# Performance work log

Hardware: AMD Instinct MI355X
Metric: run time of the kernel (lower is better)

Reference implementation:

```python
import jax, jax.numpy as jnp
import numpy as np

B = 16384
MV = 512   # movie_vector_size
UV = 512   # user_vector_size
NM = 16    # num_dense_movie_embeddings
NU = 16    # num_dense_user_embeddings
DS = 16    # dense_embedding_size
MLP = [256, 128, 1]


def setup_inputs() -> dict:
    key = jax.random.key(0)
    ks = jax.random.split(key, 12)
    inp = {
        'movie_vectors': jax.random.normal(ks[0], (B, MV), jnp.float32),
        'user_vectors': jax.random.normal(ks[1], (B, UV), jnp.float32),
        # embedding towers: Linear(in, DS*N + 1), stored as [in, out]
        'Wm': jax.random.normal(ks[2], (MV, DS * NM + 1), jnp.float32) * (1.0 / np.sqrt(MV)),
        'bm': jax.random.normal(ks[3], (DS * NM + 1,), jnp.float32) * 0.01,
        'Wu': jax.random.normal(ks[4], (UV, DS * NU + 1), jnp.float32) * (1.0 / np.sqrt(UV)),
        'bu': jax.random.normal(ks[5], (DS * NU + 1,), jnp.float32) * 0.01,
    }
    d_in = (NM + NU) * DS  # 512
    dims = [d_in] + MLP
    for i in range(len(MLP)):
        inp[f'W{i+1}'] = jax.random.normal(ks[6 + 2*i], (dims[i], dims[i+1]), jnp.float32) * (1.0 / np.sqrt(dims[i]))
        inp[f'b{i+1}'] = jax.random.normal(ks[7 + 2*i], (dims[i+1],), jnp.float32) * 0.01
    return inp


def reference(movie_vectors, user_vectors, Wm, bm, Wu, bu, W1, b1, W2, b2, W3, b3):
    batch = movie_vectors.shape[0]
    movie_dense = movie_vectors @ Wm + bm          # [B, DS*NM+1]
    user_dense = user_vectors @ Wu + bu            # [B, DS*NU+1]
    fm_additive = movie_dense[:, -1] + user_dense[:, -1]            # [B]
    m_split = movie_dense[:, :-1].reshape(batch, NM, DS)            # [B, NM, DS]
    u_split = user_dense[:, :-1].reshape(batch, NU, DS)             # [B, NU, DS]
    fm_interactions = jnp.einsum('bik,bjk->bij', m_split, u_split).reshape(batch, -1)  # [B, NM*NU]
    all_dense = jnp.concatenate([movie_dense[:, :-1], user_dense[:, :-1]], axis=-1)    # [B, (NM+NU)*DS]
    h = jax.nn.relu(all_dense @ W1 + b1)
    h = jax.nn.relu(h @ W2 + b2)
    mlp_out = h @ W3 + b3                                           # [B, 1]
    logit = mlp_out + fm_additive[:, None] + jnp.sum(fm_interactions, axis=-1, keepdims=True)
    return logit
```

## Files before the change

kernel.cpp:

```cpp
#include <hip/hip_runtime.h>


#define NTH 1024
#define RB  64

typedef __bf16 bf16x8 __attribute__((ext_vector_type(8)));
typedef float  f32x4  __attribute__((ext_vector_type(4)));

#define WS_WMF  0
#define WS_WUF  294912
#define WS_W1F  589824
#define WS_W2F  851968
#define WS_BIAS 917504

#define BPITCH  528
#define L_BST   0
#define L_DENSE 67584
#define L_FM    133120
#define L_ADD   141824
#define L_OUT   142336
#define LDSB    142592

__device__ __forceinline__ unsigned short f2bf(float f) {
  unsigned u = __builtin_bit_cast(unsigned, f);
  u += 0x7FFFu + ((u >> 16) & 1u);
  return (unsigned short)(u >> 16);
}

__device__ __forceinline__ f32x4 mfma_bf16(bf16x8 a, bf16x8 b, f32x4 c) {
  return __builtin_amdgcn_mfma_f32_16x16x32_bf16(a, b, c, 0, 0, 0);
}

extern "C" __global__ __launch_bounds__(256) void deepfm_prep(
    const float* __restrict__ Wm, const float* __restrict__ bm,
    const float* __restrict__ Wu, const float* __restrict__ bu,
    const float* __restrict__ W1, const float* __restrict__ W2,
    const float* __restrict__ b3, char* __restrict__ ws) {
  const int unit = blockIdx.x * 4 + (threadIdx.x >> 6);
  if (unit >= 897) return;
  const int l = threadIdx.x & 63;
  const int fi = l & 15, q = l >> 4;
  unsigned short h[8];
  if (unit < 576) {
    const int t = unit / 288, rem = unit % 288;
    const int kg = rem / 18, ft = rem % 18;
    const float* W = t ? Wu : Wm;
    char* outp = ws + (t ? WS_WUF : WS_WMF);
    const int f = ft * 16 + fi;
#pragma unroll
    for (int e = 0; e < 8; ++e) {
      const int k = kg * 32 + q * 8 + e;
      float val;
      if (f < 256) val = W[k * 257 + f];
      else if (f < 272) {
        float s = 0.f;
#pragma unroll
        for (int i = 0; i < 16; ++i) s += W[k * 257 + i * 16 + (f - 256)];
        val = s;
      } else if (f == 272) val = W[k * 257 + 256];
      else val = 0.f;
      h[e] = f2bf(val);
    }
    uint4 o;
    o.x = h[0] | ((unsigned)h[1] << 16); o.y = h[2] | ((unsigned)h[3] << 16);
    o.z = h[4] | ((unsigned)h[5] << 16); o.w = h[6] | ((unsigned)h[7] << 16);
    *(uint4*)(outp + (((kg * 18 + ft) * 64 + l) << 4)) = o;
  } else if (unit < 832) {
    const int bb = unit - 576;
    const int kg = bb / 16, ft = bb % 16;
    const int f = ft * 16 + fi;
#pragma unroll
    for (int e = 0; e < 8; ++e) h[e] = f2bf(W1[(kg * 32 + q * 8 + e) * 256 + f]);
    uint4 o;
    o.x = h[0] | ((unsigned)h[1] << 16); o.y = h[2] | ((unsigned)h[3] << 16);
    o.z = h[4] | ((unsigned)h[5] << 16); o.w = h[6] | ((unsigned)h[7] << 16);
    *(uint4*)(ws + WS_W1F + (((kg * 16 + ft) * 64 + l) << 4)) = o;
  } else if (unit < 896) {
    const int bb = unit - 832;
    const int kg = bb / 8, ft = bb % 8;
    const int f = ft * 16 + fi;
#pragma unroll
    for (int e = 0; e < 8; ++e) h[e] = f2bf(W2[(kg * 32 + q * 8 + e) * 128 + f]);
    uint4 o;
    o.x = h[0] | ((unsigned)h[1] << 16); o.y = h[2] | ((unsigned)h[3] << 16);
    o.z = h[4] | ((unsigned)h[5] << 16); o.w = h[6] | ((unsigned)h[7] << 16);
    *(uint4*)(ws + WS_W2F + (((kg * 8 + ft) * 64 + l) << 4)) = o;
  } else {
    float* aux = (float*)(ws + WS_BIAS);
    if (l < 16) {
      float s = 0.f;
      for (int i = 0; i < 16; ++i) s += bm[i * 16 + l];
      aux[l] = s;
    } else if (l < 32) {
      const int k = l - 16;
      float s = 0.f;
      for (int i = 0; i < 16; ++i) s += bu[i * 16 + k];
      aux[l] = s;
    } else if (l == 32) {
      aux[32] = bm[256] + bu[256] + b3[0];
    }
  }
}

extern "C" __global__ __launch_bounds__(NTH)
__attribute__((amdgpu_waves_per_eu(4, 4))) void deepfm_main(
    const float* __restrict__ movie, const float* __restrict__ user,
    const float* __restrict__ bm, const float* __restrict__ bu,
    const float* __restrict__ b1, const float* __restrict__ b2,
    const float* __restrict__ W3, const char* __restrict__ ws,
    float* __restrict__ out) {
  extern __shared__ __align__(16) char lds[];
  char* const bstage    = lds + L_BST;
  char* const densefrag = lds + L_DENSE;
  char* const h1frag    = lds + L_BST;
  float* const fmbuf    = (float*)(lds + L_FM);
  float* const addbuf   = (float*)(lds + L_ADD);
  float* const outpart  = (float*)(lds + L_OUT);

  const int tid = threadIdx.x;
  const int w   = tid >> 6;
  const int l   = tid & 63;
  const int cn  = l & 15;
  const int q   = l >> 4;
  const int row0 = blockIdx.x * RB;

  const int tw   = w >> 3;
  const int wi   = w & 7;
  const int axi  = wi & 1;
  const int axrt = wi >> 1;
  const int ftw  = w & 7;
  const int rth  = w >> 3;

  const int rot  = (int)blockIdx.x >> 3;
  const int hord = rot & 1;
  const int kk0  = (rot >> 1) & 7;
  const int p2r  = rot & 15;
  const int p3r  = rot & 7;

  const f32x4 zz = {0.f, 0.f, 0.f, 0.f};
  const float* auxb = (const float*)(ws + WS_BIAS);

  bf16x8 p2a;
  bf16x8 p3a;

  {
    const char* WF = ws + (tw ? WS_WUF : WS_WMF);
    const char* brow = bstage + tw * 64 * BPITCH;
    f32x4 a0r0 = zz, a0r1 = zz, a0r2 = zz, a0r3 = zz;
    f32x4 a1r0 = zz, a1r1 = zz, a1r2 = zz, a1r3 = zz;
    f32x4 axc = zz;

    const int h0 = hord, h1h = hord ^ 1;

#pragma unroll
    for (int p = 0; p < 8; ++p) {
      const int idx = p * 1024 + tid;
      const int rr = idx >> 6, f4 = idx & 63;
      const float* src = (rr >= 64) ? user : movie;
      const float4 v = *(const float4*)(src + (size_t)(row0 + (rr & 63)) * 512 +
                                        h0 * 256 + f4 * 4);
      uint2 o;
      o.x = f2bf(v.x) | ((unsigned)f2bf(v.y) << 16);
      o.y = f2bf(v.z) | ((unsigned)f2bf(v.w) << 16);
      *(uint2*)(bstage + rr * BPITCH + f4 * 8) = o;
    }
    __syncthreads();

    float4 pf[8];
#pragma unroll
    for (int p = 0; p < 8; ++p) {
      const int idx = p * 1024 + tid;
      const int rr = idx >> 6, f4 = idx & 63;
      const float* src = (rr >= 64) ? user : movie;
      pf[p] = *(const float4*)(src + (size_t)(row0 + (rr & 63)) * 512 +
                               h1h * 256 + f4 * 4);
    }
    uint2 pfc[8];

#pragma unroll
    for (int i = 0; i < 8; ++i) {
      const int kgl = (kk0 + i) & 7;
      const int kg  = h0 * 8 + kgl;
      const bf16x8 bf0 = *(const bf16x8*)(brow + cn * BPITCH + kgl * 64 + q * 16);
      const bf16x8 bf1 = *(const bf16x8*)(brow + (16 + cn) * BPITCH + kgl * 64 + q * 16);
      const bf16x8 bf2 = *(const bf16x8*)(brow + (32 + cn) * BPITCH + kgl * 64 + q * 16);
      const bf16x8 bf3 = *(const bf16x8*)(brow + (48 + cn) * BPITCH + kgl * 64 + q * 16);
      const bf16x8 A0 = *(const bf16x8*)(WF + (((kg * 18 + wi * 2 + 0) * 64 + l) << 4));
      const bf16x8 A1 = *(const bf16x8*)(WF + (((kg * 18 + wi * 2 + 1) * 64 + l) << 4));
      const bf16x8 AX = *(const bf16x8*)(WF + (((kg * 18 + 16 + axi) * 64 + l) << 4));
      __builtin_amdgcn_s_setprio(1);
      a0r0 = mfma_bf16(A0, bf0, a0r0);  a0r1 = mfma_bf16(A0, bf1, a0r1);
      a0r2 = mfma_bf16(A0, bf2, a0r2);  a0r3 = mfma_bf16(A0, bf3, a0r3);
      a1r0 = mfma_bf16(A1, bf0, a1r0);  a1r1 = mfma_bf16(A1, bf1, a1r1);
      a1r2 = mfma_bf16(A1, bf2, a1r2);  a1r3 = mfma_bf16(A1, bf3, a1r3);
      const bf16x8 bsel = (axrt == 0) ? bf0 : (axrt == 1) ? bf1
                        : (axrt == 2) ? bf2 : bf3;
      axc = mfma_bf16(AX, bsel, axc);
      __builtin_amdgcn_s_setprio(0);
      if (i >= 1) {
        const int j = i - 1;
        pfc[j].x = f2bf(pf[j].x) | ((unsigned)f2bf(pf[j].y) << 16);
        pfc[j].y = f2bf(pf[j].z) | ((unsigned)f2bf(pf[j].w) << 16);
      }
    }
    pfc[7].x = f2bf(pf[7].x) | ((unsigned)f2bf(pf[7].y) << 16);
    pfc[7].y = f2bf(pf[7].z) | ((unsigned)f2bf(pf[7].w) << 16);

    __syncthreads();

    bf16x8 A0c = *(const bf16x8*)(WF + ((((h1h * 8 + kk0) * 18 + wi * 2 + 0) * 64 + l) << 4));
    bf16x8 A1c = *(const bf16x8*)(WF + ((((h1h * 8 + kk0) * 18 + wi * 2 + 1) * 64 + l) << 4));

#pragma unroll
    for (int p = 0; p < 8; ++p) {
      const int idx = p * 1024 + tid;
      const int rr = idx >> 6, f4 = idx & 63;
      *(uint2*)(bstage + rr * BPITCH + f4 * 8) = pfc[p];
    }
    __syncthreads();

#pragma unroll
    for (int i = 0; i < 8; ++i) {
      const int kgl = (kk0 + i) & 7;
      const int kg  = h1h * 8 + kgl;
      const bf16x8 bf0 = *(const bf16x8*)(brow + cn * BPITCH + kgl * 64 + q * 16);
      const bf16x8 bf1 = *(const bf16x8*)(brow + (16 + cn) * BPITCH + kgl * 64 + q * 16);
      const bf16x8 bf2 = *(const bf16x8*)(brow + (32 + cn) * BPITCH + kgl * 64 + q * 16);
      const bf16x8 bf3 = *(const bf16x8*)(brow + (48 + cn) * BPITCH + kgl * 64 + q * 16);
      const bf16x8 AX = *(const bf16x8*)(WF + (((kg * 18 + 16 + axi) * 64 + l) << 4));
      bf16x8 A0n, A1n;
      if (i < 7) {
        const int nkg = h1h * 8 + ((kk0 + i + 1) & 7);
        A0n = *(const bf16x8*)(WF + (((nkg * 18 + wi * 2 + 0) * 64 + l) << 4));
        A1n = *(const bf16x8*)(WF + (((nkg * 18 + wi * 2 + 1) * 64 + l) << 4));
      } else {
        A0n = A0c; A1n = A1c;
      }
      __builtin_amdgcn_s_setprio(1);
      a0r0 = mfma_bf16(A0c, bf0, a0r0);  a0r1 = mfma_bf16(A0c, bf1, a0r1);
      a0r2 = mfma_bf16(A0c, bf2, a0r2);  a0r3 = mfma_bf16(A0c, bf3, a0r3);
      a1r0 = mfma_bf16(A1c, bf0, a1r0);  a1r1 = mfma_bf16(A1c, bf1, a1r1);
      a1r2 = mfma_bf16(A1c, bf2, a1r2);  a1r3 = mfma_bf16(A1c, bf3, a1r3);
      const bf16x8 bsel = (axrt == 0) ? bf0 : (axrt == 1) ? bf1
                        : (axrt == 2) ? bf2 : bf3;
      axc = mfma_bf16(AX, bsel, axc);
      __builtin_amdgcn_s_setprio(0);
      A0c = A0n; A1c = A1n;
    }

    p2a = *(const bf16x8*)(ws + WS_W1F + (((p2r * 16 + w) * 64 + l) << 4));

    const float* bt = tw ? bu : bm;
    const f32x4 accA[2][4] = {{a0r0, a0r1, a0r2, a0r3}, {a1r0, a1r1, a1r2, a1r3}};
#pragma unroll
    for (int s = 0; s < 2; ++s) {
      const int ft = wi * 2 + s;
      const int fb = ft * 16 + q * 4;
      const float g0 = bt[fb], g1 = bt[fb + 1], g2 = bt[fb + 2], g3 = bt[fb + 3];
      const int kd = tw * 256 + fb;
      const int kgd = kd >> 5, qd = (kd >> 3) & 3, ed = kd & 4;
#pragma unroll
      for (int rt = 0; rt < 4; ++rt) {
        const f32x4 v = accA[s][rt];
        uint2 p;
        p.x = f2bf(v[0] + g0) | ((unsigned)f2bf(v[1] + g1) << 16);
        p.y = f2bf(v[2] + g2) | ((unsigned)f2bf(v[3] + g3) << 16);
        *(uint2*)(densefrag + (((kgd * 4 + rt) * 64 + qd * 16 + cn) << 4) +
                  (ed ? 8 : 0)) = p;
      }
    }

    if (axi == 0) {
#pragma unroll
      for (int reg = 0; reg < 4; ++reg)
        fmbuf[(tw * 64 + axrt * 16 + cn) * 17 + (q * 4 + reg)] = axc[reg];
    } else if (q == 0) {
      addbuf[tw * 64 + axrt * 16 + cn] = axc[0];
    }
  }

  __syncthreads();

  if (tid < 64) {
    float p = 0.f;
#pragma unroll
    for (int k = 0; k < 16; ++k)
      p += (fmbuf[tid * 17 + k] + auxb[k]) *
           (fmbuf[(64 + tid) * 17 + k] + auxb[16 + k]);
    outpart[tid] = p + addbuf[tid] + addbuf[64 + tid] + auxb[32];
  }

  {
    const char* W1F = ws + WS_W1F;
    bf16x8 a0c = p2a;
    f32x4 r0 = zz, r1 = zz, r2 = zz, r3 = zz;
#pragma unroll
    for (int i = 0; i < 16; ++i) {
      const int kg = (p2r + i) & 15;
      const bf16x8 b0 = *(const bf16x8*)(densefrag + (((kg * 4 + 0) * 64 + l) << 4));
      const bf16x8 b1f = *(const bf16x8*)(densefrag + (((kg * 4 + 1) * 64 + l) << 4));
      const bf16x8 b2f = *(const bf16x8*)(densefrag + (((kg * 4 + 2) * 64 + l) << 4));
      const bf16x8 b3f = *(const bf16x8*)(densefrag + (((kg * 4 + 3) * 64 + l) << 4));
      bf16x8 a0n;
      if (i < 15) {
        const int nkg = (p2r + i + 1) & 15;
        a0n = *(const bf16x8*)(W1F + (((nkg * 16 + w) * 64 + l) << 4));
      } else {
        a0n = a0c;
      }
      __builtin_amdgcn_s_setprio(1);
      r0 = mfma_bf16(a0c, b0,  r0);
      r1 = mfma_bf16(a0c, b1f, r1);
      r2 = mfma_bf16(a0c, b2f, r2);
      r3 = mfma_bf16(a0c, b3f, r3);
      __builtin_amdgcn_s_setprio(0);
      a0c = a0n;
    }

    p3a = *(const bf16x8*)(ws + WS_W2F + (((p3r * 8 + ftw) * 64 + l) << 4));

    const f32x4 accA[4] = {r0, r1, r2, r3};
    const int fb = w * 16 + q * 4;
    const float g0 = b1[fb], g1 = b1[fb + 1], g2 = b1[fb + 2], g3 = b1[fb + 3];
    const int kgd = fb >> 5, qd = (fb >> 3) & 3, ed = fb & 4;
#pragma unroll
    for (int rt = 0; rt < 4; ++rt) {
      const f32x4 v = accA[rt];
      uint2 p;
      p.x = f2bf(fmaxf(v[0] + g0, 0.f)) | ((unsigned)f2bf(fmaxf(v[1] + g1, 0.f)) << 16);
      p.y = f2bf(fmaxf(v[2] + g2, 0.f)) | ((unsigned)f2bf(fmaxf(v[3] + g3, 0.f)) << 16);
      *(uint2*)(h1frag + (((kgd * 4 + rt) * 64 + qd * 16 + cn) << 4) +
                (ed ? 8 : 0)) = p;
    }
  }

  __syncthreads();

  {
    const char* W2F = ws + WS_W2F;
    bf16x8 a0c = p3a;
    f32x4 d0 = zz, d1 = zz;
#pragma unroll
    for (int i = 0; i < 8; ++i) {
      const int kg = (p3r + i) & 7;
      const bf16x8 b0 = *(const bf16x8*)(h1frag + (((kg * 4 + rth * 2 + 0) * 64 + l) << 4));
      const bf16x8 b1f = *(const bf16x8*)(h1frag + (((kg * 4 + rth * 2 + 1) * 64 + l) << 4));
      bf16x8 a0n;
      if (i < 7) {
        const int nkg = (p3r + i + 1) & 7;
        a0n = *(const bf16x8*)(W2F + (((nkg * 8 + ftw) * 64 + l) << 4));
      } else {
        a0n = a0c;
      }
      d0 = mfma_bf16(a0c, b0,  d0);
      d1 = mfma_bf16(a0c, b1f, d1);
      a0c = a0n;
    }
    const int fb = ftw * 16 + q * 4;
    float bb[4], ww[4];
#pragma unroll
    for (int i = 0; i < 4; ++i) { bb[i] = b2[fb + i]; ww[i] = W3[fb + i]; }
    const f32x4 acc3[2] = {d0, d1};
#pragma unroll
    for (int j = 0; j < 2; ++j) {
      const int rt = rth * 2 + j;
      float p = 0.f;
#pragma unroll
      for (int reg = 0; reg < 4; ++reg)
        p += fmaxf(acc3[j][reg] + bb[reg], 0.f) * ww[reg];
      p += __shfl_xor(p, 16, 64);
      p += __shfl_xor(p, 32, 64);
      if (l < 16) atomicAdd(&outpart[rt * 16 + cn], p);
    }
  }

  __syncthreads();
  if (tid < 64) out[row0 + tid] = outpart[tid];
}

extern "C" void kernel_launch(void* const* d_in, const int* in_sizes, int n_in,
                              void* d_out, int out_size, void* d_ws, size_t ws_size,
                              hipStream_t stream) {
  const float* movie = (const float*)d_in[0];
  const float* user  = (const float*)d_in[1];
  const float* Wm = (const float*)d_in[2];
  const float* bm = (const float*)d_in[3];
  const float* Wu = (const float*)d_in[4];
  const float* bu = (const float*)d_in[5];
  const float* W1 = (const float*)d_in[6];
  const float* b1 = (const float*)d_in[7];
  const float* W2 = (const float*)d_in[8];
  const float* b2 = (const float*)d_in[9];
  const float* W3 = (const float*)d_in[10];
  const float* b3 = (const float*)d_in[11];
  char* ws = (char*)d_ws;
  float* out = (float*)d_out;

  (void)hipFuncSetAttribute((const void*)deepfm_main,
                            hipFuncAttributeMaxDynamicSharedMemorySize, LDSB);

  deepfm_prep<<<225, 256, 0, stream>>>(Wm, bm, Wu, bu, W1, W2, b3, ws);
  deepfm_main<<<256, NTH, LDSB, stream>>>(movie, user, bm, bu, b1, b2, W3, ws, out);
}
```

Measured before the change: 129.8 us.

## Use nontemporal weight loads, deepen prefetch, and consolidate aux and layer-3 MFMA work into fewer waves

Weight fragment loads from the workspace now use nontemporal loads. The W1 and W2 fragment prefetch is deepened from one to two iterations ahead. The auxiliary FM/additive MFMAs are consolidated onto half the waves, each doing two row tiles, so the other waves skip those loads. The third-layer GEMM now runs on 8 waves that each cover all 4 row tiles instead of 16 waves covering 2 each. This aims to hide global latency and cut redundant weight loads, but it unbalances work across waves and raises register pressure.

```diff
diff --git a/kernel.cpp b/kernel.cpp
--- a/kernel.cpp
+++ b/kernel.cpp
@@ -29,6 +29,10 @@
 
 __device__ __forceinline__ f32x4 mfma_bf16(bf16x8 a, bf16x8 b, f32x4 c) {
   return __builtin_amdgcn_mfma_f32_16x16x32_bf16(a, b, c, 0, 0, 0);
+}
+
+__device__ __forceinline__ bf16x8 ldnt(const char* p) {
+  return __builtin_nontemporal_load((const bf16x8*)p);
 }
 
 extern "C" __global__ __launch_bounds__(256) void deepfm_prep(
@@ -127,9 +131,7 @@
   const int tw   = w >> 3;
   const int wi   = w & 7;
   const int axi  = wi & 1;
-  const int axrt = wi >> 1;
-  const int ftw  = w & 7;
-  const int rth  = w >> 3;
+  const int rtb  = (wi >> 1) * 2;
 
   const int rot  = (int)blockIdx.x >> 3;
   const int hord = rot & 1;
@@ -140,15 +142,15 @@
   const f32x4 zz = {0.f, 0.f, 0.f, 0.f};
   const float* auxb = (const float*)(ws + WS_BIAS);
 
-  bf16x8 p2a;
-  bf16x8 p3a;
+  bf16x8 p2a, p2b;
+  bf16x8 p3a, p3b;
 
   {
     const char* WF = ws + (tw ? WS_WUF : WS_WMF);
     const char* brow = bstage + tw * 64 * BPITCH;
     f32x4 a0r0 = zz, a0r1 = zz, a0r2 = zz, a0r3 = zz;
     f32x4 a1r0 = zz, a1r1 = zz, a1r2 = zz, a1r3 = zz;
-    f32x4 axc = zz;
+    f32x4 axc0 = zz, axc1 = zz;
 
     const int h0 = hord, h1h = hord ^ 1;
 
@@ -185,17 +187,21 @@
       const bf16x8 bf1 = *(const bf16x8*)(brow + (16 + cn) * BPITCH + kgl * 64 + q * 16);
       const bf16x8 bf2 = *(const bf16x8*)(brow + (32 + cn) * BPITCH + kgl * 64 + q * 16);
       const bf16x8 bf3 = *(const bf16x8*)(brow + (48 + cn) * BPITCH + kgl * 64 + q * 16);
-      const bf16x8 A0 = *(const bf16x8*)(WF + (((kg * 18 + wi * 2 + 0) * 64 + l) << 4));
-      const bf16x8 A1 = *(const bf16x8*)(WF + (((kg * 18 + wi * 2 + 1) * 64 + l) << 4));
-      const bf16x8 AX = *(const bf16x8*)(WF + (((kg * 18 + 16 + axi) * 64 + l) << 4));
+      const bf16x8 A0 = ldnt(WF + (((kg * 18 + wi * 2 + 0) * 64 + l) << 4));
+      const bf16x8 A1 = ldnt(WF + (((kg * 18 + wi * 2 + 1) * 64 + l) << 4));
+      bf16x8 AX;
+      if (wi < 4) AX = ldnt(WF + (((kg * 18 + 16 + axi) * 64 + l) << 4));
       __builtin_amdgcn_s_setprio(1);
       a0r0 = mfma_bf16(A0, bf0, a0r0);  a0r1 = mfma_bf16(A0, bf1, a0r1);
       a0r2 = mfma_bf16(A0, bf2, a0r2);  a0r3 = mfma_bf16(A0, bf3, a0r3);
       a1r0 = mfma_bf16(A1, bf0, a1r0);  a1r1 = mfma_bf16(A1, bf1, a1r1);
       a1r2 = mfma_bf16(A1, bf2, a1r2);  a1r3 = mfma_bf16(A1, bf3, a1r3);
-      const bf16x8 bsel = (axrt == 0) ? bf0 : (axrt == 1) ? bf1
-                        : (axrt == 2) ? bf2 : bf3;
-      axc = mfma_bf16(AX, bsel, axc);
+      if (wi < 4) {
+        const bf16x8 bs0 = rtb ? bf2 : bf0;
+        const bf16x8 bs1 = rtb ? bf3 : bf1;
+        axc0 = mfma_bf16(AX, bs0, axc0);
+        axc1 = mfma_bf16(AX, bs1, axc1);
+      }
       __builtin_amdgcn_s_setprio(0);
       if (i >= 1) {
         const int j = i - 1;
@@ -208,8 +214,8 @@
 
     __syncthreads();
 
-    bf16x8 A0c = *(const bf16x8*)(WF + ((((h1h * 8 + kk0) * 18 + wi * 2 + 0) * 64 + l) << 4));
-    bf16x8 A1c = *(const bf16x8*)(WF + ((((h1h * 8 + kk0) * 18 + wi * 2 + 1) * 64 + l) << 4));
+    bf16x8 A0c = ldnt(WF + ((((h1h * 8 + kk0) * 18 + wi * 2 + 0) * 64 + l) << 4));
+    bf16x8 A1c = ldnt(WF + ((((h1h * 8 + kk0) * 18 + wi * 2 + 1) * 64 + l) << 4));
 
 #pragma unroll
     for (int p = 0; p < 8; ++p) {
@@ -227,12 +233,13 @@
       const bf16x8 bf1 = *(const bf16x8*)(brow + (16 + cn) * BPITCH + kgl * 64 + q * 16);
       const bf16x8 bf2 = *(const bf16x8*)(brow + (32 + cn) * BPITCH + kgl * 64 + q * 16);
       const bf16x8 bf3 = *(const bf16x8*)(brow + (48 + cn) * BPITCH + kgl * 64 + q * 16);
-      const bf16x8 AX = *(const bf16x8*)(WF + (((kg * 18 + 16 + axi) * 64 + l) << 4));
+      bf16x8 AX;
+      if (wi < 4) AX = ldnt(WF + (((kg * 18 + 16 + axi) * 64 + l) << 4));
       bf16x8 A0n, A1n;
       if (i < 7) {
         const int nkg = h1h * 8 + ((kk0 + i + 1) & 7);
-        A0n = *(const bf16x8*)(WF + (((nkg * 18 + wi * 2 + 0) * 64 + l) << 4));
-        A1n = *(const bf16x8*)(WF + (((nkg * 18 + wi * 2 + 1) * 64 + l) << 4));
+        A0n = ldnt(WF + (((nkg * 18 + wi * 2 + 0) * 64 + l) << 4));
+        A1n = ldnt(WF + (((nkg * 18 + wi * 2 + 1) * 64 + l) << 4));
       } else {
         A0n = A0c; A1n = A1c;
       }
@@ -241,14 +248,18 @@
       a0r2 = mfma_bf16(A0c, bf2, a0r2);  a0r3 = mfma_bf16(A0c, bf3, a0r3);
       a1r0 = mfma_bf16(A1c, bf0, a1r0);  a1r1 = mfma_bf16(A1c, bf1, a1r1);
       a1r2 = mfma_bf16(A1c, bf2, a1r2);  a1r3 = mfma_bf16(A1c, bf3, a1r3);
-      const bf16x8 bsel = (axrt == 0) ? bf0 : (axrt == 1) ? bf1
-                        : (axrt == 2) ? bf2 : bf3;
-      axc = mfma_bf16(AX, bsel, axc);
+      if (wi < 4) {
+        const bf16x8 bs0 = rtb ? bf2 : bf0;
+        const bf16x8 bs1 = rtb ? bf3 : bf1;
+        axc0 = mfma_bf16(AX, bs0, axc0);
+        axc1 = mfma_bf16(AX, bs1, axc1);
+      }
       __builtin_amdgcn_s_setprio(0);
       A0c = A0n; A1c = A1n;
     }
 
-    p2a = *(const bf16x8*)(ws + WS_W1F + (((p2r * 16 + w) * 64 + l) << 4));
+    p2a = ldnt(ws + WS_W1F + (((p2r * 16 + w) * 64 + l) << 4));
+    p2b = ldnt(ws + WS_W1F + (((((p2r + 1) & 15) * 16 + w) * 64 + l) << 4));
 
     const float* bt = tw ? bu : bm;
     const f32x4 accA[2][4] = {{a0r0, a0r1, a0r2, a0r3}, {a1r0, a1r1, a1r2, a1r3}};
@@ -270,12 +281,17 @@
       }
     }
 
-    if (axi == 0) {
-#pragma unroll
-      for (int reg = 0; reg < 4; ++reg)
-        fmbuf[(tw * 64 + axrt * 16 + cn) * 17 + (q * 4 + reg)] = axc[reg];
-    } else if (q == 0) {
-      addbuf[tw * 64 + axrt * 16 + cn] = axc[0];
+    if (wi < 4) {
+      if (axi == 0) {
+#pragma unroll
+        for (int reg = 0; reg < 4; ++reg) {
+          fmbuf[(tw * 64 + rtb * 16 + cn) * 17 + (q * 4 + reg)] = axc0[reg];
+          fmbuf[(tw * 64 + (rtb + 1) * 16 + cn) * 17 + (q * 4 + reg)] = axc1[reg];
+        }
+      } else if (q == 0) {
+        addbuf[tw * 64 + rtb * 16 + cn] = axc0[0];
+        addbuf[tw * 64 + (rtb + 1) * 16 + cn] = axc1[0];
+      }
     }
   }
 
@@ -293,6 +309,7 @@
   {
     const char* W1F = ws + WS_W1F;
     bf16x8 a0c = p2a;
+    bf16x8 a0n = p2b;
     f32x4 r0 = zz, r1 = zz, r2 = zz, r3 = zz;
 #pragma unroll
     for (int i = 0; i < 16; ++i) {
@@ -301,12 +318,10 @@
       const bf16x8 b1f = *(const bf16x8*)(densefrag + (((kg * 4 + 1) * 64 + l) << 4));
       const bf16x8 b2f = *(const bf16x8*)(densefrag + (((kg * 4 + 2) * 64 + l) << 4));
       const bf16x8 b3f = *(const bf16x8*)(densefrag + (((kg * 4 + 3) * 64 + l) << 4));
-      bf16x8 a0n;
-      if (i < 15) {
-        const int nkg = (p2r + i + 1) & 15;
-        a0n = *(const bf16x8*)(W1F + (((nkg * 16 + w) * 64 + l) << 4));
-      } else {
-        a0n = a0c;
+      bf16x8 a2;
+      if (i < 14) {
+        const int nkg = (p2r + i + 2) & 15;
+        a2 = ldnt(W1F + (((nkg * 16 + w) * 64 + l) << 4));
       }
       __builtin_amdgcn_s_setprio(1);
       r0 = mfma_bf16(a0c, b0,  r0);
@@ -315,9 +330,13 @@
       r3 = mfma_bf16(a0c, b3f, r3);
       __builtin_amdgcn_s_setprio(0);
       a0c = a0n;
-    }
-
-    p3a = *(const bf16x8*)(ws + WS_W2F + (((p3r * 8 + ftw) * 64 + l) << 4));
+      if (i < 14) a0n = a2;
+    }
+
+    if (w < 8) {
+      p3a = ldnt(ws + WS_W2F + (((p3r * 8 + w) * 64 + l) << 4));
+      p3b = ldnt(ws + WS_W2F + (((((p3r + 1) & 7) * 8 + w) * 64 + l) << 4));
+    }
 
     const f32x4 accA[4] = {r0, r1, r2, r3};
     const int fb = w * 16 + q * 4;
@@ -336,41 +355,44 @@
 
   __syncthreads();
 
-  {
+  if (w < 8) {
     const char* W2F = ws + WS_W2F;
     bf16x8 a0c = p3a;
-    f32x4 d0 = zz, d1 = zz;
+    bf16x8 a0n = p3b;
+    f32x4 d0 = zz, d1 = zz, d2 = zz, d3 = zz;
 #pragma unroll
     for (int i = 0; i < 8; ++i) {
       const int kg = (p3r + i) & 7;
-      const bf16x8 b0 = *(const bf16x8*)(h1frag + (((kg * 4 + rth * 2 + 0) * 64 + l) << 4));
-      const bf16x8 b1f = *(const bf16x8*)(h1frag + (((kg * 4 + rth * 2 + 1) * 64 + l) << 4));
-      bf16x8 a0n;
-      if (i < 7) {
-        const int nkg = (p3r + i + 1) & 7;
-        a0n = *(const bf16x8*)(W2F + (((nkg * 8 + ftw) * 64 + l) << 4));
-      } else {
-        a0n = a0c;
+      const bf16x8 b0 = *(const bf16x8*)(h1frag + (((kg * 4 + 0) * 64 + l) << 4));
+      const bf16x8 b1f = *(const bf16x8*)(h1frag + (((kg * 4 + 1) * 64 + l) << 4));
+      const bf16x8 b2f = *(const bf16x8*)(h1frag + (((kg * 4 + 2) * 64 + l) << 4));
+      const bf16x8 b3f = *(const bf16x8*)(h1frag + (((kg * 4 + 3) * 64 + l) << 4));
+      bf16x8 a2;
+      if (i < 6) {
+        const int nkg = (p3r + i + 2) & 7;
+        a2 = ldnt(W2F + (((nkg * 8 + w) * 64 + l) << 4));
       }
       d0 = mfma_bf16(a0c, b0,  d0);
       d1 = mfma_bf16(a0c, b1f, d1);
+      d2 = mfma_bf16(a0c, b2f, d2);
+      d3 = mfma_bf16(a0c, b3f, d3);
       a0c = a0n;
-    }
-    const int fb = ftw * 16 + q * 4;
+      if (i < 6) a0n = a2;
+    }
+    const int fb = w * 16 + q * 4;
     float bb[4], ww[4];
 #pragma unroll
     for (int i = 0; i < 4; ++i) { bb[i] = b2[fb + i]; ww[i] = W3[fb + i]; }
-    const f32x4 acc3[2] = {d0, d1};
-#pragma unroll
-    for (int j = 0; j < 2; ++j) {
-      const int rt = rth * 2 + j;
+    const f32x4 acc3[4] = {d0, d1, d2, d3};
+#pragma unroll
+    for (int j = 0; j < 4; ++j) {
       float p = 0.f;
 #pragma unroll
       for (int reg = 0; reg < 4; ++reg)
         p += fmaxf(acc3[j][reg] + bb[reg], 0.f) * ww[reg];
       p += __shfl_xor(p, 16, 64);
       p += __shfl_xor(p, 32, 64);
-      if (l < 16) atomicAdd(&outpart[rt * 16 + cn], p);
+      if (l < 16) atomicAdd(&outpart[j * 16 + cn], p);
     }
   }
 
```

After: 135.2 us. 1.04x slower.
